# Kernel optimization log

Measured on AMD Instinct MI355X. Metric: run time of the kernel, lower is better.

## Reference

```python
import jax, jax.numpy as jnp
import numpy as np

DIM = 768
HEADS = 12
DIM_HEAD = 64
INNER = HEADS * DIM_HEAD  # 768
SCALE = DIM_HEAD ** -0.5
LN_EPS = 1e-5


def setup_inputs() -> dict:
    key = jax.random.key(0)
    ks = jax.random.split(key, 6)
    B, N = 2, 1024
    x = jax.random.normal(ks[0], (B, N, DIM), dtype=jnp.float32)
    ln_g = jnp.ones((DIM,), jnp.float32)
    ln_b = jnp.zeros((DIM,), jnp.float32)
    # torch nn.Linear weights are [out, in]
    w_qkv = jax.random.normal(ks[1], (3 * INNER, DIM), jnp.float32) * (DIM ** -0.5)
    w_out = jax.random.normal(ks[2], (DIM, INNER), jnp.float32) * (INNER ** -0.5)
    b_out = jnp.zeros((DIM,), jnp.float32)
    theta = jax.random.normal(ks[3], (HEADS, HEADS), jnp.float32)
    # xavier_uniform for 12x12
    lim = float(np.sqrt(6.0 / (HEADS + HEADS)))
    gnn_w = jax.random.uniform(ks[4], (HEADS, HEADS), jnp.float32, -lim, lim)
    return {"x": x, "ln_g": ln_g, "ln_b": ln_b, "w_qkv": w_qkv,
            "w_out": w_out, "b_out": b_out, "theta": theta, "gnn_w": gnn_w}


def _dc_crd(attn, theta, gnn_w):
    # attn: [B, H, N, N] treated as image with H=12 channels
    B, H, N, _ = attn.shape
    w = attn.mean(axis=(-2, -1))  # adaptive_avg_pool2d -> [B, H]
    diff = w[:, :, None] - w[:, None, :]  # [B, H, H]
    # abs(1 - exp(-d)/(1+exp(-d))) - 1 == abs(1 - sigmoid(-d)) - 1
    T_w = jnp.abs(1.0 - jax.nn.sigmoid(-diff)) - 1.0
    adj = (T_w + jnp.swapaxes(T_w, -1, -2)) * 0.5 * theta  # [B, H, H]
    attn_flat = attn.reshape(B, H, N * N)
    support = jnp.einsum('ij,bjm->bim', gnn_w, attn_flat)  # W @ features
    out = jax.nn.relu(jnp.einsum('bij,bjm->bim', adj, support))  # spmm(adj, support)
    return out.reshape(B, H, N, N)


def reference(x, ln_g, ln_b, w_qkv, w_out, b_out, theta, gnn_w):
    B, N, D = x.shape
    mu = x.mean(-1, keepdims=True)
    var = x.var(-1, keepdims=True)
    xn = (x - mu) * jax.lax.rsqrt(var + LN_EPS) * ln_g + ln_b
    qkv = xn @ w_qkv.T  # [B, N, 3*INNER]
    q, k, v = jnp.split(qkv, 3, axis=-1)
    def heads(t):
        return t.reshape(B, N, HEADS, DIM_HEAD).transpose(0, 2, 1, 3)
    q, k, v = heads(q), heads(k), heads(v)  # [B, H, N, d]
    dots = jnp.einsum('bhnd,bhmd->bhnm', q, k) * SCALE
    attn = jax.nn.softmax(dots, axis=-1)
    H = _dc_crd(attn, theta, gnn_w)
    out = jnp.einsum('bhnm,bhmd->bhnd', attn + H, v)
    out = out.transpose(0, 2, 1, 3).reshape(B, N, INNER)
    return out @ w_out.T + b_out
```

## Files before the change

### kernel.cpp

```cpp
#include <hip/hip_runtime.h>
#include <hip/hip_bf16.h>
#include <stdint.h>

#define NB 2
#define SEQ 1024
#define DMODEL 768
#define NH 12
#define DH 64
#define SCALE 0.125f
#define NCH 4

typedef __hip_bfloat16 bf16;
typedef __attribute__((ext_vector_type(8))) short short8;
typedef __attribute__((ext_vector_type(4))) float f32x4;

__device__ __forceinline__ bf16 f2b(float x){ return __float2bfloat16(x); }
__device__ __forceinline__ short f2bs(float x){
  bf16 h = __float2bfloat16(x); return *reinterpret_cast<short*>(&h);
}
__device__ __forceinline__ float s2f(short u){
  return __uint_as_float(((unsigned)(unsigned short)u) << 16);
}

__device__ __forceinline__ void gl_lds16(const bf16* g, bf16* l){
  __builtin_amdgcn_global_load_lds(
      (const __attribute__((address_space(1))) void*)g,
      (__attribute__((address_space(3))) void*)l, 16, 0, 0);
}

__global__ __launch_bounds__(256) void prep_all(const float* __restrict__ x,
                                                const float* __restrict__ g,
                                                const float* __restrict__ bta,
                                                const float* __restrict__ w1, int n1,
                                                const float* __restrict__ w2, int n2,
                                                const float* __restrict__ theta,
                                                const float* __restrict__ gnn,
                                                bf16* __restrict__ xn,
                                                bf16* __restrict__ wb,
                                                float* __restrict__ Mm,
                                                float* __restrict__ l){
  int bx = blockIdx.x, t = threadIdx.x;
  if (bx < 2048){
    const float* xr = x + (size_t)bx*DMODEL;
    float v0[3]; float s = 0.f, s2 = 0.f;
    #pragma unroll
    for (int i=0;i<3;i++){ float val = xr[t+256*i]; v0[i]=val; s+=val; s2+=val*val; }
    __shared__ float sb[256], s2b[256];
    sb[t]=s; s2b[t]=s2; __syncthreads();
    for (int off=128; off>0; off>>=1){
      if (t<off){ sb[t]+=sb[t+off]; s2b[t]+=s2b[t+off]; }
      __syncthreads();
    }
    float mean = sb[0]*(1.f/DMODEL);
    float var  = s2b[0]*(1.f/DMODEL) - mean*mean;
    float rstd = rsqrtf(var + 1e-5f);
    #pragma unroll
    for (int i=0;i<3;i++){
      int c = t+256*i;
      xn[(size_t)bx*DMODEL + c] = f2b((v0[i]-mean)*rstd*g[c] + bta[c]);
    }
  } else if (bx < 2048+9216){
    int i = (bx-2048)*256 + t;
    if (i < n1) wb[i] = f2b(w1[i]);
    else if (i < n1+n2) wb[i] = f2b(w2[i-n1]);
  } else {
    int sub = bx - (2048+9216);
    if (sub == 0){
      if (t < 144){
        int i = t/12, kx = t%12;
        float sacc = 0.f;
        for (int j=0;j<12;j++) sacc += (-0.5f)*theta[i*12+j] * gnn[j*12+kx];
        Mm[t] = sacc;
      }
    } else {
      l[(sub-1)*256 + t] = 0.f;
    }
  }
}

__global__ __launch_bounds__(256) void gemm_qkv(const bf16* __restrict__ A,
                                                const bf16* __restrict__ W,
                                                bf16* __restrict__ q,
                                                bf16* __restrict__ k,
                                                bf16* __restrict__ vt){
  __shared__ bf16 As[128*32];
  __shared__ bf16 Bs[128*32];
  int n0 = blockIdx.x*128, m0 = blockIdx.y*128;
  int t = threadIdx.x, w = t>>6, lane = t&63;
  int ln16 = lane&15, q8 = (lane>>4)*8;
  int wm = w>>1, wn = w&1;
  f32x4 acc[4][4] = {};
  for (int k0=0; k0<768; k0+=32){
    __syncthreads();
    #pragma unroll
    for (int i=0;i<2;i++){
      int cc = t + i*256;
      int r = cc>>2, ko = (cc&3)*8;
      gl_lds16(&A[(size_t)(m0+r)*768 + k0+ko], &As[(size_t)(w*64 + i*256)*8]);
      gl_lds16(&W[(size_t)(n0+r)*768 + k0+ko], &Bs[(size_t)(w*64 + i*256)*8]);
    }
    __syncthreads();
    short8 af[4], bfr[4];
    #pragma unroll
    for (int mi=0;mi<4;mi++) af[mi]  = *(const short8*)&As[(wm*64+mi*16+ln16)*32 + q8];
    #pragma unroll
    for (int ni=0;ni<4;ni++) bfr[ni] = *(const short8*)&Bs[(wn*64+ni*16+ln16)*32 + q8];
    #pragma unroll
    for (int mi=0;mi<4;mi++)
      #pragma unroll
      for (int ni=0;ni<4;ni++)
        acc[mi][ni] = __builtin_amdgcn_mfma_f32_16x16x32_bf16(af[mi], bfr[ni], acc[mi][ni], 0, 0, 0);
  }
  int quad4 = (lane>>4)*4;
  #pragma unroll
  for (int mi=0;mi<4;mi++){
    #pragma unroll
    for (int ni=0;ni<4;ni++){
      int cg = n0 + wn*64 + ni*16 + ln16;
      int which = cg/768; int rem = cg - which*768;
      int h = rem>>6, dd = rem&63;
      #pragma unroll
      for (int r=0;r<4;r++){
        int m = m0 + wm*64 + mi*16 + quad4 + r;
        int bb = m>>10, n = m&1023;
        float val = acc[mi][ni][r];
        if (which==0)      q [((size_t)(bb*NH+h)*SEQ + n)*DH + dd] = f2b(val*SCALE);
        else if (which==1) k [((size_t)(bb*NH+h)*SEQ + n)*DH + dd] = f2b(val);
        else               vt[((size_t)(bb*NH+h)*DH + dd)*SEQ + n] = f2b(val);
      }
    }
  }
}

__global__ __launch_bounds__(768) void attn_sums(const bf16* __restrict__ q,
                                                 const bf16* __restrict__ k,
                                                 float* __restrict__ l){
  int b = blockIdx.z, ch = blockIdx.y; int r0 = blockIdx.x*16;
  int t = threadIdx.x; int h = t>>6; int lane = t&63;
  int ln16 = lane&15, quad = lane>>4; int q8 = quad*8, quad4 = quad*4;
  const bf16* qrow = q + ((size_t)(b*NH+h)*SEQ + r0 + ln16)*DH;
  short8 aq0 = *(const short8*)(qrow + q8);
  short8 aq1 = *(const short8*)(qrow + 32 + q8);
  const bf16* kB = k + ((size_t)(b*NH+h)*SEQ)*DH;
  float ls[4] = {0.f,0.f,0.f,0.f};
  #pragma unroll 4
  for (int i=0;i<16;i++){
    int c0 = ch*256 + i*16;
    const bf16* krow = kB + (size_t)(c0 + ln16)*DH;
    short8 bk0 = *(const short8*)(krow + q8);
    short8 bk1 = *(const short8*)(krow + 32 + q8);
    f32x4 a = {0.f,0.f,0.f,0.f};
    a = __builtin_amdgcn_mfma_f32_16x16x32_bf16(aq0, bk0, a, 0, 0, 0);
    a = __builtin_amdgcn_mfma_f32_16x16x32_bf16(aq1, bk1, a, 0, 0, 0);
    #pragma unroll
    for (int r=0;r<4;r++) ls[r] += __expf(a[r]);
  }
  #pragma unroll
  for (int msk=1; msk<16; msk<<=1){
    #pragma unroll
    for (int r=0;r<4;r++) ls[r] += __shfl_xor(ls[r], msk);
  }
  if (ln16 == 0){
    #pragma unroll
    for (int r=0;r<4;r++)
      atomicAdd(&l[((size_t)(b*NH+h))*SEQ + r0 + quad4 + r], ls[r]);
  }
}

__global__ __launch_bounds__(768) void attn_main(const bf16* __restrict__ q,
                                                 const bf16* __restrict__ k,
                                                 const bf16* __restrict__ vt,
                                                 const float* __restrict__ Mm,
                                                 const float* __restrict__ l,
                                                 bf16* __restrict__ opart){
  __shared__ bf16 attT[2][NH][16][40];
  __shared__ float Ms[144];
  int b = blockIdx.z, ch = blockIdx.y; int r0 = blockIdx.x*16;
  int t = threadIdx.x; int h = t>>6; int lane = t&63;
  int ln16 = lane&15, quad = lane>>4; int q8 = quad*8, quad4 = quad*4;
  const bf16* kB = k  + ((size_t)(b*NH+h)*SEQ)*DH;
  const bf16* vB = vt + ((size_t)(b*NH+h)*DH)*SEQ;

  if (t < 144) Ms[t] = Mm[t];

  const bf16* qrow = q + ((size_t)(b*NH+h)*SEQ + r0 + ln16)*DH;
  short8 aq0 = *(const short8*)(qrow + q8);
  short8 aq1 = *(const short8*)(qrow + 32 + q8);

  float inv_l[4];
  #pragma unroll
  for (int r=0;r<4;r++) inv_l[r] = 1.0f / l[((size_t)(b*NH+h))*SEQ + r0 + quad4 + r];

  f32x4 oacc[4] = {};
  for (int it=0; it<8; it++){
    int c0 = ch*256 + it*32;
    int buf = it&1;
    #pragma unroll
    for (int half=0; half<2; half++){
      const bf16* krow = kB + (size_t)(c0 + half*16 + ln16)*DH;
      short8 bk0 = *(const short8*)(krow + q8);
      short8 bk1 = *(const short8*)(krow + 32 + q8);
      f32x4 a = {0.f,0.f,0.f,0.f};
      a = __builtin_amdgcn_mfma_f32_16x16x32_bf16(aq0, bk0, a, 0, 0, 0);
      a = __builtin_amdgcn_mfma_f32_16x16x32_bf16(aq1, bk1, a, 0, 0, 0);
      #pragma unroll
      for (int r=0;r<4;r++)
        attT[buf][h][quad4+r][half*16 + ln16] = f2b(__expf(a[r])*inv_l[r]);
    }
    __syncthreads();
    float sm[8] = {0.f,0.f,0.f,0.f,0.f,0.f,0.f,0.f};
    #pragma unroll
    for (int j=0;j<12;j++){
      short8 u = *(const short8*)&attT[buf][j][ln16][q8];
      float m = Ms[h*12+j];
      #pragma unroll
      for (int e=0;e<8;e++) sm[e] += m*s2f(u[e]);
    }
    short8 uh = *(const short8*)&attT[buf][h][ln16][q8];
    short8 afrag;
    #pragma unroll
    for (int e=0;e<8;e++) afrag[e] = f2bs(s2f(uh[e]) + fmaxf(sm[e], 0.f));
    #pragma unroll
    for (int ni=0; ni<4; ni++){
      short8 bv = *(const short8*)&vB[(size_t)(ni*16 + ln16)*SEQ + c0 + q8];
      oacc[ni] = __builtin_amdgcn_mfma_f32_16x16x32_bf16(afrag, bv, oacc[ni], 0, 0, 0);
    }
  }
  bf16* dst = opart + ((size_t)ch*NB*SEQ + (size_t)b*SEQ)*DMODEL;
  #pragma unroll
  for (int ni=0; ni<4; ni++)
    #pragma unroll
    for (int r=0; r<4; r++){
      int n = r0 + quad4 + r;
      dst[(size_t)n*DMODEL + h*DH + ni*16 + ln16] = f2b(oacc[ni][r]);
    }
}

__global__ __launch_bounds__(256) void reduce_kernel(const bf16* __restrict__ opart,
                                                     bf16* __restrict__ aout){
  const size_t TOT = (size_t)NB*SEQ*DMODEL;
  size_t i = ((size_t)blockIdx.x*256 + threadIdx.x)*8;
  float s[8] = {};
  #pragma unroll
  for (int c=0;c<NCH;c++){
    short8 u = *(const short8*)&opart[c*TOT + i];
    #pragma unroll
    for (int e=0;e<8;e++) s[e] += s2f(u[e]);
  }
  short8 o;
  #pragma unroll
  for (int e=0;e<8;e++) o[e] = f2bs(s[e]);
  *(short8*)&aout[i] = o;
}

__global__ __launch_bounds__(256) void gemm_out(const bf16* __restrict__ A,
                                                const bf16* __restrict__ W,
                                                const float* __restrict__ bias,
                                                float* __restrict__ out){
  __shared__ bf16 As[64*32];
  __shared__ bf16 Bs[64*32];
  int n0 = blockIdx.x*64, m0 = blockIdx.y*64;
  int t = threadIdx.x, w = t>>6, lane = t&63;
  int ln16 = lane&15, q8 = (lane>>4)*8;
  int wm = w>>1, wn = w&1;
  f32x4 acc[2][2] = {};
  for (int k0=0; k0<768; k0+=32){
    __syncthreads();
    {
      int r = t>>2, ko = (t&3)*8;
      gl_lds16(&A[(size_t)(m0+r)*768 + k0+ko], &As[(size_t)(w*64)*8]);
      gl_lds16(&W[(size_t)(n0+r)*768 + k0+ko], &Bs[(size_t)(w*64)*8]);
    }
    __syncthreads();
    short8 af[2], bfr[2];
    #pragma unroll
    for (int mi=0;mi<2;mi++) af[mi]  = *(const short8*)&As[(wm*32+mi*16+ln16)*32 + q8];
    #pragma unroll
    for (int ni=0;ni<2;ni++) bfr[ni] = *(const short8*)&Bs[(wn*32+ni*16+ln16)*32 + q8];
    #pragma unroll
    for (int mi=0;mi<2;mi++)
      #pragma unroll
      for (int ni=0;ni<2;ni++)
        acc[mi][ni] = __builtin_amdgcn_mfma_f32_16x16x32_bf16(af[mi], bfr[ni], acc[mi][ni], 0, 0, 0);
  }
  int quad4 = (lane>>4)*4;
  #pragma unroll
  for (int mi=0;mi<2;mi++)
    #pragma unroll
    for (int ni=0;ni<2;ni++){
      int cg = n0 + wn*32 + ni*16 + ln16;
      #pragma unroll
      for (int r=0;r<4;r++){
        int m = m0 + wm*32 + mi*16 + quad4 + r;
        out[(size_t)m*768 + cg] = acc[mi][ni][r] + bias[cg];
      }
    }
}

extern "C" void kernel_launch(void* const* d_in, const int* in_sizes, int n_in,
                              void* d_out, int out_size, void* d_ws, size_t ws_size,
                              hipStream_t stream){
  const float* x     = (const float*)d_in[0];
  const float* ln_g  = (const float*)d_in[1];
  const float* ln_b  = (const float*)d_in[2];
  const float* w_qkv = (const float*)d_in[3];
  const float* w_out = (const float*)d_in[4];
  const float* b_out = (const float*)d_in[5];
  const float* theta = (const float*)d_in[6];
  const float* gnn   = (const float*)d_in[7];
  float* out = (float*)d_out;

  char* p = (char*)d_ws;
  bf16* xnb   = (bf16*)p; p += (size_t)2048*768*2;
  bf16* wqkvb = (bf16*)p; p += (size_t)2304*768*2;
  bf16* woutb = (bf16*)p; p += (size_t)768*768*2;
  bf16* qb    = (bf16*)p; p += (size_t)NB*NH*SEQ*DH*2;
  bf16* kb    = (bf16*)p; p += (size_t)NB*NH*SEQ*DH*2;
  bf16* vtb   = (bf16*)p; p += (size_t)NB*NH*SEQ*DH*2;
  bf16* aoutb = (bf16*)p; p += (size_t)2048*768*2;
  float* Mm   = (float*)p; p += 256*4;
  float* lsum = (float*)p; p += (size_t)NB*NH*SEQ*4;
  bf16* opart = (bf16*)p;

  const int N1 = 2304*768, N2 = 768*768;
  prep_all<<<dim3(2048+9216+97), dim3(256), 0, stream>>>(
      x, ln_g, ln_b, w_qkv, N1, w_out, N2, theta, gnn, xnb, wqkvb, Mm, lsum);
  gemm_qkv<<<dim3(18, 16), dim3(256), 0, stream>>>(xnb, wqkvb, qb, kb, vtb);
  attn_sums<<<dim3(64, NCH, NB), dim3(768), 0, stream>>>(qb, kb, lsum);
  attn_main<<<dim3(64, NCH, NB), dim3(768), 0, stream>>>(qb, kb, vtb, Mm, lsum, opart);
  reduce_kernel<<<dim3(NB*SEQ*DMODEL/(8*256)), dim3(256), 0, stream>>>(opart, aoutb);
  gemm_out<<<dim3(12, 32), dim3(256), 0, stream>>>(aoutb, woutb, b_out, out);
}
```

Baseline: 199.2 us.

## Compute head-mixing matmul with MFMA using split hi/lo bf16 mixing matrix

The scalar 12x12 head-mixing step in attn_main, which read each head's attention tile from LDS and did FMA loops, now runs on MFMA instructions. The mixing matrix is stored as a padded 32-wide bf16 pair (high and low parts) to keep near-fp32 accuracy. Attention values are laid out head-contiguous in a new LDS buffer, and combined results go into a second buffer that feeds the PV MFMA. This adds an extra __syncthreads per iteration, drops the double buffering, and uses more LDS, which could lower occupancy.

```diff
diff --git a/kernel.cpp b/kernel.cpp
--- a/kernel.cpp
+++ b/kernel.cpp
@@ -10,8 +10,12 @@
 #define SCALE 0.125f
 #define NCH 4
 
+#define AJ_RS 1288
+#define CT_HS 648
+
 typedef __hip_bfloat16 bf16;
 typedef __attribute__((ext_vector_type(8))) short short8;
+typedef __attribute__((ext_vector_type(2))) short s2v;
 typedef __attribute__((ext_vector_type(4))) float f32x4;
 
 __device__ __forceinline__ bf16 f2b(float x){ return __float2bfloat16(x); }
@@ -37,7 +41,7 @@
                                                 const float* __restrict__ gnn,
                                                 bf16* __restrict__ xn,
                                                 bf16* __restrict__ wb,
-                                                float* __restrict__ Mm,
+                                                bf16* __restrict__ Mb,
                                                 float* __restrict__ l){
   int bx = blockIdx.x, t = threadIdx.x;
   if (bx < 2048){
@@ -66,11 +70,17 @@
   } else {
     int sub = bx - (2048+9216);
     if (sub == 0){
-      if (t < 144){
-        int i = t/12, kx = t%12;
+      #pragma unroll
+      for (int e=0;e<2;e++){
+        int idx = t + 256*e;
+        int i = idx >> 5, j = idx & 31;
         float sacc = 0.f;
-        for (int j=0;j<12;j++) sacc += (-0.5f)*theta[i*12+j] * gnn[j*12+kx];
-        Mm[t] = sacc;
+        if (i < 12 && j < 12)
+          for (int jj=0;jj<12;jj++) sacc += (-0.5f)*theta[i*12+jj] * gnn[jj*12+j];
+        bf16 hi = f2b(sacc);
+        float lo = sacc - __bfloat162float(hi);
+        Mb[idx]       = hi;
+        Mb[512 + idx] = f2b(lo);
       }
     } else {
       l[(sub-1)*256 + t] = 0.f;
@@ -170,18 +180,22 @@
 __global__ __launch_bounds__(768) void attn_main(const bf16* __restrict__ q,
                                                  const bf16* __restrict__ k,
                                                  const bf16* __restrict__ vt,
-                                                 const float* __restrict__ Mm,
+                                                 const bf16* __restrict__ Mb,
                                                  const float* __restrict__ l,
                                                  bf16* __restrict__ opart){
-  __shared__ bf16 attT[2][NH][16][40];
-  __shared__ float Ms[144];
+  __shared__ __align__(16) bf16 attJ[16*AJ_RS];
+  __shared__ __align__(16) bf16 combT[16*CT_HS];
   int b = blockIdx.z, ch = blockIdx.y; int r0 = blockIdx.x*16;
   int t = threadIdx.x; int h = t>>6; int lane = t&63;
   int ln16 = lane&15, quad = lane>>4; int q8 = quad*8, quad4 = quad*4;
   const bf16* kB = k  + ((size_t)(b*NH+h)*SEQ)*DH;
   const bf16* vB = vt + ((size_t)(b*NH+h)*DH)*SEQ;
 
-  if (t < 144) Ms[t] = Mm[t];
+  short8 z8 = (short8){0,0,0,0,0,0,0,0};
+  for (int i = t*8; i < 16*AJ_RS; i += 768*8) *(short8*)&attJ[i] = z8;
+
+  short8 mhi = *(const short8*)&Mb[ln16*32 + q8];
+  short8 mlo = *(const short8*)&Mb[512 + ln16*32 + q8];
 
   const bf16* qrow = q + ((size_t)(b*NH+h)*SEQ + r0 + ln16)*DH;
   short8 aq0 = *(const short8*)(qrow + q8);
@@ -191,10 +205,11 @@
   #pragma unroll
   for (int r=0;r<4;r++) inv_l[r] = 1.0f / l[((size_t)(b*NH+h))*SEQ + r0 + quad4 + r];
 
+  __syncthreads();
+
   f32x4 oacc[4] = {};
   for (int it=0; it<8; it++){
     int c0 = ch*256 + it*32;
-    int buf = it&1;
     #pragma unroll
     for (int half=0; half<2; half++){
       const bf16* krow = kB + (size_t)(c0 + half*16 + ln16)*DH;
@@ -203,23 +218,29 @@
       f32x4 a = {0.f,0.f,0.f,0.f};
       a = __builtin_amdgcn_mfma_f32_16x16x32_bf16(aq0, bk0, a, 0, 0, 0);
       a = __builtin_amdgcn_mfma_f32_16x16x32_bf16(aq1, bk1, a, 0, 0, 0);
+      int cc = half*16 + ln16;
       #pragma unroll
       for (int r=0;r<4;r++)
-        attT[buf][h][quad4+r][half*16 + ln16] = f2b(__expf(a[r])*inv_l[r]);
-    }
-    __syncthreads();
-    float sm[8] = {0.f,0.f,0.f,0.f,0.f,0.f,0.f,0.f};
-    #pragma unroll
-    for (int j=0;j<12;j++){
-      short8 u = *(const short8*)&attT[buf][j][ln16][q8];
-      float m = Ms[h*12+j];
-      #pragma unroll
-      for (int e=0;e<8;e++) sm[e] += m*s2f(u[e]);
-    }
-    short8 uh = *(const short8*)&attT[buf][h][ln16][q8];
-    short8 afrag;
-    #pragma unroll
-    for (int e=0;e<8;e++) afrag[e] = f2bs(s2f(uh[e]) + fmaxf(sm[e], 0.f));
+        attJ[(quad4+r)*AJ_RS + cc*40 + h] = f2b(__expf(a[r])*inv_l[r]);
+    }
+    __syncthreads();
+    for (int tl = h; tl < 32; tl += 12){
+      int n = tl*16 + ln16;
+      int base = (n>>5)*AJ_RS + (n&31)*40;
+      short8 bfrag = *(const short8*)&attJ[base + q8];
+      f32x4 c = {0.f,0.f,0.f,0.f};
+      c = __builtin_amdgcn_mfma_f32_16x16x32_bf16(mlo, bfrag, c, 0, 0, 0);
+      c = __builtin_amdgcn_mfma_f32_16x16x32_bf16(mhi, bfrag, c, 0, 0, 0);
+      s2v id01 = *(const s2v*)&attJ[base + quad4];
+      s2v id23 = *(const s2v*)&attJ[base + quad4 + 2];
+      float idf[4] = { s2f(id01[0]), s2f(id01[1]), s2f(id23[0]), s2f(id23[1]) };
+      int cbase = (n>>5)*40 + (n&31);
+      #pragma unroll
+      for (int ri=0; ri<4; ri++)
+        combT[(quad4+ri)*CT_HS + cbase] = f2b(idf[ri] + fmaxf(c[ri], 0.f));
+    }
+    __syncthreads();
+    short8 afrag = *(const short8*)&combT[h*CT_HS + ln16*40 + q8];
     #pragma unroll
     for (int ni=0; ni<4; ni++){
       short8 bv = *(const short8*)&vB[(size_t)(ni*16 + ln16)*SEQ + c0 + q8];
@@ -318,16 +339,16 @@
   bf16* kb    = (bf16*)p; p += (size_t)NB*NH*SEQ*DH*2;
   bf16* vtb   = (bf16*)p; p += (size_t)NB*NH*SEQ*DH*2;
   bf16* aoutb = (bf16*)p; p += (size_t)2048*768*2;
-  float* Mm   = (float*)p; p += 256*4;
+  bf16* Mbw   = (bf16*)p; p += (size_t)1024*2;
   float* lsum = (float*)p; p += (size_t)NB*NH*SEQ*4;
   bf16* opart = (bf16*)p;
 
   const int N1 = 2304*768, N2 = 768*768;
   prep_all<<<dim3(2048+9216+97), dim3(256), 0, stream>>>(
-      x, ln_g, ln_b, w_qkv, N1, w_out, N2, theta, gnn, xnb, wqkvb, Mm, lsum);
+      x, ln_g, ln_b, w_qkv, N1, w_out, N2, theta, gnn, xnb, wqkvb, Mbw, lsum);
   gemm_qkv<<<dim3(18, 16), dim3(256), 0, stream>>>(xnb, wqkvb, qb, kb, vtb);
   attn_sums<<<dim3(64, NCH, NB), dim3(768), 0, stream>>>(qb, kb, lsum);
-  attn_main<<<dim3(64, NCH, NB), dim3(768), 0, stream>>>(qb, kb, vtb, Mm, lsum, opart);
+  attn_main<<<dim3(64, NCH, NB), dim3(768), 0, stream>>>(qb, kb, vtb, Mbw, lsum, opart);
   reduce_kernel<<<dim3(NB*SEQ*DMODEL/(8*256)), dim3(256), 0, stream>>>(opart, aoutb);
   gemm_out<<<dim3(12, 32), dim3(256), 0, stream>>>(aoutb, woutb, b_out, out);
 }
```

Measured after the change: 202.0 us. No clear change (+1.4%).
